# Optimization experiments

Hardware: AMD Instinct MI355X
Metric: run time of the kernel (lower is better)

The kernel has to match this reference:

```python
import jax, jax.numpy as jnp
import numpy as np

N_NODES = 100000
N_EDGES = 3200000
NUM_GRAPHS = 128
DIM = 2


def setup_inputs() -> dict:
    key = jax.random.key(0)
    k1, k2, k3 = jax.random.split(key, 3)
    node_pos = jax.random.normal(k1, (N_NODES, DIM), dtype=jnp.float32)
    raw_edge_index = jax.random.randint(k2, (2, N_EDGES), 0, N_NODES, dtype=jnp.int64)
    batch = jnp.sort(jax.random.randint(k3, (N_NODES,), 0, NUM_GRAPHS, dtype=jnp.int64))
    return {"node_pos": node_pos, "raw_edge_index": raw_edge_index, "batch": batch}


def reference(node_pos, raw_edge_index, batch):
    # gather edge endpoints: [E, DIM]
    start = node_pos[raw_edge_index[0]]
    end = node_pos[raw_edge_index[1]]
    # per-edge (||end - start|| - 1)^2 : [E]
    eu = jnp.linalg.norm(end - start, axis=1)
    edge_var = jnp.square(eu - 1.0)
    # graph id of each edge (via its source node): [E]
    index = batch[raw_edge_index[0]]
    # scatter-mean by graph
    sums = jax.ops.segment_sum(edge_var, index, num_segments=NUM_GRAPHS)
    counts = jax.ops.segment_sum(jnp.ones_like(edge_var), index, num_segments=NUM_GRAPHS)
    graph_var = sums / jnp.maximum(counts, 1.0)
    # self.reduce defaults to torch.mean over graphs -> scalar
    return jnp.mean(graph_var)
```

## Files before the change

### kernel.cpp

```cpp
#include <hip/hip_runtime.h>

#define NGRAPH 128
#define NBLK   512
#define BS     256

__global__ __launch_bounds__(BS) void edgevar_stage1(
    const float* __restrict__ pos,
    const int*   __restrict__ ei,
    const int*   __restrict__ batch,
    float*       __restrict__ part,
    int E) {
  __shared__ float s_acc[2 * NGRAPH];
  for (int i = threadIdx.x; i < 2 * NGRAPH; i += BS) s_acc[i] = 0.f;
  __syncthreads();

  const int tid = blockIdx.x * BS + threadIdx.x;
  const int nth = NBLK * BS;
  const int E4  = E >> 2;
  const int4*   __restrict__ s4 = (const int4*)ei;
  const int4*   __restrict__ d4 = (const int4*)(ei + E);
  const float2* __restrict__ p2 = (const float2*)pos;

  for (int i = tid; i < E4; i += nth) {
    int4 s = s4[i];
    int4 d = d4[i];
    int ss[4] = {s.x, s.y, s.z, s.w};
    int dd[4] = {d.x, d.y, d.z, d.w};
#pragma unroll
    for (int k = 0; k < 4; ++k) {
      float2 a = p2[ss[k]];
      float2 b = p2[dd[k]];
      float dx = b.x - a.x, dy = b.y - a.y;
      float eu = sqrtf(dx * dx + dy * dy);
      float v  = eu - 1.f;
      v *= v;
      int g = batch[ss[k]];
      atomicAdd(&s_acc[g], v);
      atomicAdd(&s_acc[NGRAPH + g], 1.f);
    }
  }
  for (int e = (E4 << 2) + tid; e < E; e += nth) {
    int sn = ei[e];
    int dn = ei[e + E];
    float2 a = p2[sn];
    float2 b = p2[dn];
    float dx = b.x - a.x, dy = b.y - a.y;
    float eu = sqrtf(dx * dx + dy * dy);
    float v  = eu - 1.f;
    v *= v;
    int g = batch[sn];
    atomicAdd(&s_acc[g], v);
    atomicAdd(&s_acc[NGRAPH + g], 1.f);
  }

  __syncthreads();
  float* dst = part + (size_t)blockIdx.x * (2 * NGRAPH);
  for (int i = threadIdx.x; i < 2 * NGRAPH; i += BS) dst[i] = s_acc[i];
}

__global__ __launch_bounds__(2 * NGRAPH) void edgevar_stage2(
    const float* __restrict__ part,
    float*       __restrict__ out) {
  const int t = threadIdx.x;
  float acc = 0.f;
#pragma unroll 8
  for (int b = 0; b < NBLK; ++b) acc += part[(size_t)b * (2 * NGRAPH) + t];

  __shared__ float s[2 * NGRAPH];
  s[t] = acc;
  __syncthreads();

  __shared__ float red[NGRAPH];
  if (t < NGRAPH) {
    float sum = s[t];
    float cnt = s[NGRAPH + t];
    red[t] = sum / fmaxf(cnt, 1.f);
  }
  __syncthreads();
  if (t < 64) {
    float v = red[t] + red[t + 64];
    for (int off = 32; off; off >>= 1) v += __shfl_down(v, off);
    if (t == 0) out[0] = v * (1.0f / NGRAPH);
  }
}

extern "C" void kernel_launch(void* const* d_in, const int* in_sizes, int n_in,
                              void* d_out, int out_size, void* d_ws, size_t ws_size,
                              hipStream_t stream) {
  const float* pos   = (const float*)d_in[0];
  const int*   ei    = (const int*)d_in[1];
  const int*   batch = (const int*)d_in[2];
  float*       out   = (float*)d_out;
  float*       part  = (float*)d_ws;
  const int E = in_sizes[1] / 2;

  hipLaunchKernelGGL(edgevar_stage1, dim3(NBLK), dim3(BS), 0, stream,
                     pos, ei, batch, part, E);
  hipLaunchKernelGGL(edgevar_stage2, dim3(1), dim3(2 * NGRAPH), 0, stream,
                     part, out);
}
```

Baseline: 131.6 us.

## Pack node position and graph id into float4; reduce partials via global atomics

Adds a pre-pass that packs each node's position and batch id into one 16-byte record, so each edge's source lookup is a single gather instead of two separate gathers. The grid grows from 512 to 2048 blocks. Per-block partials now go into one global accumulator through atomics instead of a buffer that a single-block kernel summed serially, which shortens finalize to a tiny kernel. In exchange it adds an extra kernel launch, a pass over all nodes, and more atomic contention on the global accumulator.

Result: slower. 142.3 us (+8.1%).

```diff
diff --git a/kernel.cpp b/kernel.cpp
--- a/kernel.cpp
+++ b/kernel.cpp
@@ -1,25 +1,39 @@
 #include <hip/hip_runtime.h>
 
 #define NGRAPH 128
-#define NBLK   512
+#define NBLK   2048
 #define BS     256
 
+
+__global__ __launch_bounds__(BS) void edgevar_pack(
+    const float2* __restrict__ pos,
+    const int*    __restrict__ batch,
+    float4*       __restrict__ packed,
+    float*        __restrict__ acc,
+    int N) {
+  const int i = blockIdx.x * BS + threadIdx.x;
+  if (blockIdx.x == 0 && threadIdx.x < 2 * NGRAPH) acc[threadIdx.x] = 0.f;
+  if (i < N) {
+    float2 p = pos[i];
+    packed[i] = make_float4(p.x, p.y, __int_as_float(batch[i]), 0.f);
+  }
+}
+
 __global__ __launch_bounds__(BS) void edgevar_stage1(
-    const float* __restrict__ pos,
-    const int*   __restrict__ ei,
-    const int*   __restrict__ batch,
-    float*       __restrict__ part,
+    const float4* __restrict__ packed,
+    const int*    __restrict__ ei,
+    float*        __restrict__ acc,
     int E) {
   __shared__ float s_acc[2 * NGRAPH];
-  for (int i = threadIdx.x; i < 2 * NGRAPH; i += BS) s_acc[i] = 0.f;
+  if (threadIdx.x < 2 * NGRAPH) s_acc[threadIdx.x] = 0.f;
   __syncthreads();
 
   const int tid = blockIdx.x * BS + threadIdx.x;
   const int nth = NBLK * BS;
   const int E4  = E >> 2;
-  const int4*   __restrict__ s4 = (const int4*)ei;
-  const int4*   __restrict__ d4 = (const int4*)(ei + E);
-  const float2* __restrict__ p2 = (const float2*)pos;
+  const int4*   __restrict__ s4  = (const int4*)ei;
+  const int4*   __restrict__ d4  = (const int4*)(ei + E);
+  const float2* __restrict__ pp2 = (const float2*)packed;
 
   for (int i = tid; i < E4; i += nth) {
     int4 s = s4[i];
@@ -28,74 +42,62 @@
     int dd[4] = {d.x, d.y, d.z, d.w};
 #pragma unroll
     for (int k = 0; k < 4; ++k) {
-      float2 a = p2[ss[k]];
-      float2 b = p2[dd[k]];
+      float4 a = packed[ss[k]];
+      float2 b = pp2[2 * dd[k]];
       float dx = b.x - a.x, dy = b.y - a.y;
       float eu = sqrtf(dx * dx + dy * dy);
       float v  = eu - 1.f;
       v *= v;
-      int g = batch[ss[k]];
+      int g = __float_as_int(a.z);
       atomicAdd(&s_acc[g], v);
       atomicAdd(&s_acc[NGRAPH + g], 1.f);
     }
   }
   for (int e = (E4 << 2) + tid; e < E; e += nth) {
-    int sn = ei[e];
-    int dn = ei[e + E];
-    float2 a = p2[sn];
-    float2 b = p2[dn];
+    float4 a = packed[ei[e]];
+    float2 b = pp2[2 * ei[e + E]];
     float dx = b.x - a.x, dy = b.y - a.y;
     float eu = sqrtf(dx * dx + dy * dy);
     float v  = eu - 1.f;
     v *= v;
-    int g = batch[sn];
+    int g = __float_as_int(a.z);
     atomicAdd(&s_acc[g], v);
     atomicAdd(&s_acc[NGRAPH + g], 1.f);
   }
 
   __syncthreads();
-  float* dst = part + (size_t)blockIdx.x * (2 * NGRAPH);
-  for (int i = threadIdx.x; i < 2 * NGRAPH; i += BS) dst[i] = s_acc[i];
+  if (threadIdx.x < 2 * NGRAPH) {
+    float v = s_acc[threadIdx.x];
+    atomicAdd(&acc[threadIdx.x], v);
+  }
 }
 
-__global__ __launch_bounds__(2 * NGRAPH) void edgevar_stage2(
-    const float* __restrict__ part,
+__global__ __launch_bounds__(64) void edgevar_finalize(
+    const float* __restrict__ acc,
     float*       __restrict__ out) {
   const int t = threadIdx.x;
-  float acc = 0.f;
-#pragma unroll 8
-  for (int b = 0; b < NBLK; ++b) acc += part[(size_t)b * (2 * NGRAPH) + t];
-
-  __shared__ float s[2 * NGRAPH];
-  s[t] = acc;
-  __syncthreads();
-
-  __shared__ float red[NGRAPH];
-  if (t < NGRAPH) {
-    float sum = s[t];
-    float cnt = s[NGRAPH + t];
-    red[t] = sum / fmaxf(cnt, 1.f);
-  }
-  __syncthreads();
-  if (t < 64) {
-    float v = red[t] + red[t + 64];
-    for (int off = 32; off; off >>= 1) v += __shfl_down(v, off);
-    if (t == 0) out[0] = v * (1.0f / NGRAPH);
-  }
+  float v = acc[t]      / fmaxf(acc[128 + t], 1.f)
+          + acc[t + 64] / fmaxf(acc[192 + t], 1.f);
+  for (int off = 32; off; off >>= 1) v += __shfl_down(v, off);
+  if (t == 0) out[0] = v * (1.0f / NGRAPH);
 }
 
 extern "C" void kernel_launch(void* const* d_in, const int* in_sizes, int n_in,
                               void* d_out, int out_size, void* d_ws, size_t ws_size,
                               hipStream_t stream) {
-  const float* pos   = (const float*)d_in[0];
-  const int*   ei    = (const int*)d_in[1];
-  const int*   batch = (const int*)d_in[2];
-  float*       out   = (float*)d_out;
-  float*       part  = (float*)d_ws;
+  const float2* pos   = (const float2*)d_in[0];
+  const int*    ei    = (const int*)d_in[1];
+  const int*    batch = (const int*)d_in[2];
+  float*        out   = (float*)d_out;
+  float*        acc    = (float*)d_ws;
+  float4*       packed = (float4*)((char*)d_ws + 1024);
+  const int N = in_sizes[0] / 2;
   const int E = in_sizes[1] / 2;
 
+  hipLaunchKernelGGL(edgevar_pack, dim3((N + BS - 1) / BS), dim3(BS), 0, stream,
+                     pos, batch, packed, acc, N);
   hipLaunchKernelGGL(edgevar_stage1, dim3(NBLK), dim3(BS), 0, stream,
-                     pos, ei, batch, part, E);
-  hipLaunchKernelGGL(edgevar_stage2, dim3(1), dim3(2 * NGRAPH), 0, stream,
-                     part, out);
+                     packed, ei, acc, E);
+  hipLaunchKernelGGL(edgevar_finalize, dim3(1), dim3(64), 0, stream,
+                     acc, out);
 }
```
